# Optimization experiments

Measured on AMD Instinct MI355X. Metric: run time of the kernel, lower is better.

The kernel has to match this reference:

```python
import jax, jax.numpy as jnp
import numpy as np

B, K, D, S, E = 256, 512, 64, 100000, 20000  # batch, knowledge_n, low_dim, student_n, exer_n


def setup_inputs() -> dict:
    key = jax.random.key(0)
    ks = jax.random.split(key, 10)
    stu_id = jax.random.randint(ks[0], (B,), 0, S)
    exer_id = jax.random.randint(ks[1], (B,), 0, E)
    kn_emb = jax.random.uniform(ks[2], (B, K), dtype=jnp.float32)
    # learned parameters (xavier-ish scale)
    stu_table = jax.random.normal(ks[3], (S, D), dtype=jnp.float32) * 0.05
    exer_table = jax.random.normal(ks[4], (E, D), dtype=jnp.float32) * 0.05
    kn_table = jax.random.normal(ks[5], (K, D), dtype=jnp.float32) * 0.05
    W1 = jax.random.normal(ks[6], (K, K + D), dtype=jnp.float32) * (2.0 / (2 * K + D)) ** 0.5
    W2 = jax.random.normal(ks[7], (K, K + D), dtype=jnp.float32) * (2.0 / (2 * K + D)) ** 0.5
    W3 = jax.random.normal(ks[8], (1, K), dtype=jnp.float32) * (2.0 / (K + 1)) ** 0.5
    b3 = jnp.zeros((1,), dtype=jnp.float32)
    return {"stu_id": stu_id, "exer_id": exer_id, "kn_emb": kn_emb,
            "stu_table": stu_table, "exer_table": exer_table, "kn_table": kn_table,
            "W1": W1, "W2": W2, "W3": W3, "b3": b3}


def reference(stu_id, exer_id, kn_emb, stu_table, exer_table, kn_table, W1, W2, W3, b3):
    k = kn_table.shape[0]  # knowledge_n
    # sigmoid(stu_emb @ kn_table.T): (B, K) per-concept proficiency / difficulty
    stu = jax.nn.sigmoid(stu_table[stu_id] @ kn_table.T)
    exer = jax.nn.sigmoid(exer_table[exer_id] @ kn_table.T)
    # Linear on cat([repeated stu/exer vec, kn_vector]) decomposes: split W into
    # the first K columns (acting on the batch vector, constant over the K axis)
    # and the last D columns (acting on kn_table, constant over batch).
    pref = jax.nn.sigmoid((stu @ W1[:, :k].T)[:, None, :] + (kn_table @ W1[:, k:].T)[None, :, :])  # (B,K,K)
    diff = jax.nn.sigmoid((exer @ W2[:, :k].T)[:, None, :] + (kn_table @ W2[:, k:].T)[None, :, :])  # (B,K,K)
    o = jax.nn.sigmoid(jnp.einsum('bkn,n->bk', pref - diff, W3[0]) + b3)  # (B,K)
    sum_out = jnp.sum(o * kn_emb, axis=1, keepdims=True)  # (B,1)
    count = jnp.sum(kn_emb, axis=1, keepdims=True)
    return sum_out / count
```

## Files before the change

kernel.cpp:

```cpp
#include <hip/hip_runtime.h>

#define B_ 256
#define K_ 512
#define D_ 64
#define KD_ 576
#define LOG2E 1.44269504088896340736f

typedef float v2f __attribute__((ext_vector_type(2)));
typedef float v4f __attribute__((ext_vector_type(4)));
typedef short bf16x8 __attribute__((ext_vector_type(8)));
typedef float f32x16 __attribute__((ext_vector_type(16)));

#define ZERO16 {0.f,0.f,0.f,0.f,0.f,0.f,0.f,0.f,0.f,0.f,0.f,0.f,0.f,0.f,0.f,0.f}

__device__ __forceinline__ float fexp2(float x) {
#if __has_builtin(__builtin_amdgcn_exp2f)
    return __builtin_amdgcn_exp2f(x);
#else
    float r; asm("v_exp_f32 %0, %1" : "=v"(r) : "v"(x)); return r;
#endif
}
__device__ __forceinline__ float frcp(float x) {
#if __has_builtin(__builtin_amdgcn_rcpf)
    return __builtin_amdgcn_rcpf(x);
#else
    float r; asm("v_rcp_f32 %0, %1" : "=v"(r) : "v"(x)); return r;
#endif
}
__device__ __forceinline__ float fsig(float x) {
    return frcp(1.0f + fexp2(-LOG2E * x));
}
__device__ __forceinline__ ushort f2bf(float f) {
    union { float f; unsigned u; } v; v.f = f;
    return (ushort)((v.u + 0x7FFFu + ((v.u >> 16) & 1u)) >> 16);
}
__device__ __forceinline__ bf16x8 ldcvt8(const float* p) {
    float4 a = *(const float4*)p;
    float4 b = *(const float4*)(p + 4);
    bf16x8 r;
    r[0] = (short)f2bf(a.x); r[1] = (short)f2bf(a.y);
    r[2] = (short)f2bf(a.z); r[3] = (short)f2bf(a.w);
    r[4] = (short)f2bf(b.x); r[5] = (short)f2bf(b.y);
    r[6] = (short)f2bf(b.z); r[7] = (short)f2bf(b.w);
    return r;
}

__global__ void __launch_bounds__(256) kSF(const int* __restrict__ sid,
                                           const int* __restrict__ eid,
                                           const float* __restrict__ stu_t,
                                           const float* __restrict__ exer_t,
                                           const float* __restrict__ kn_t,
                                           const float* __restrict__ W1,
                                           const float* __restrict__ W2,
                                           ushort* __restrict__ Sbu,
                                           float* __restrict__ FT1,
                                           float* __restrict__ FT2) {
    __shared__ float shm[64 * 65];
    const int bid = blockIdx.x, t = threadIdx.x;
    const int l = t & 63, w = t >> 6;
    const int dk = (l >> 5) * 8;
    if (bid < 64) {
        const int tab = bid >> 5, bt = (bid >> 3) & 3, nt = bid & 7;
        const int b0 = bt * 64, n0 = nt * 64;
        const int brow = b0 + (w & 1) * 32 + (l & 31);
        const int ncol = n0 + (w >> 1) * 32 + (l & 31);
        const int id = (tab ? eid : sid)[brow];
        const float* ar = (tab ? exer_t : stu_t) + (size_t)id * D_;
        const float* br = kn_t + (size_t)ncol * D_;
        f32x16 acc = ZERO16;
#pragma unroll
        for (int kk = 0; kk < 4; kk++) {
            bf16x8 a = ldcvt8(ar + kk * 16 + dk);
            bf16x8 b = ldcvt8(br + kk * 16 + dk);
            acc = __builtin_amdgcn_mfma_f32_32x32x16_bf16(a, b, acc, 0, 0, 0);
        }
        ushort* So = Sbu + (size_t)tab * B_ * K_;
#pragma unroll
        for (int r = 0; r < 16; r++) {
            const int row = (r & 3) + 8 * (r >> 2) + 4 * (l >> 5);
            So[(size_t)(b0 + (w & 1) * 32 + row) * K_ + ncol] = f2bf(fsig(acc[r]));
        }
    } else {
        const int fid = bid - 64;
        const int mat = fid >> 6, kt = (fid >> 3) & 7, nt = fid & 7;
        const int k0 = kt * 64, n0 = nt * 64;
        const int krow = k0 + (w & 1) * 32 + (l & 31);
        const int ncol = n0 + (w >> 1) * 32 + (l & 31);
        const float* Wm = mat ? W2 : W1;
        const float* ar = kn_t + (size_t)krow * D_;
        const float* br = Wm + (size_t)ncol * KD_ + K_;
        f32x16 acc = ZERO16;
#pragma unroll
        for (int kk = 0; kk < 4; kk++) {
            bf16x8 a = ldcvt8(ar + kk * 16 + dk);
            bf16x8 b = ldcvt8(br + kk * 16 + dk);
            acc = __builtin_amdgcn_mfma_f32_32x32x16_bf16(a, b, acc, 0, 0, 0);
        }
        const int nl_ = (w >> 1) * 32 + (l & 31);
#pragma unroll
        for (int r = 0; r < 16; r++) {
            const int row = (r & 3) + 8 * (r >> 2) + 4 * (l >> 5);
            shm[nl_ * 65 + (w & 1) * 32 + row] = fexp2(-LOG2E * acc[r]);
        }
        __syncthreads();
        float* Fo = mat ? FT2 : FT1;
#pragma unroll
        for (int i = 0; i < 16; i++) {
            const int q = i * 256 + t;
            const int r_ = q >> 6, c_ = q & 63;
            Fo[(size_t)(n0 + r_) * K_ + k0 + c_] = shm[r_ * 65 + c_];
        }
    }
}

__global__ void __launch_bounds__(256) kE(const ushort* __restrict__ Sbu,
                                          const float* __restrict__ W1,
                                          const float* __restrict__ W2,
                                          float* __restrict__ E) {
    __shared__ float shm[4224];
    const int bid = blockIdx.x, t = threadIdx.x;
    const int l = t & 63, w = t >> 6;
    const int mat = bid >> 7, bt = (bid >> 4) & 7, nt = bid & 15;
    const int b0 = bt * 32, n0 = nt * 32;
    const int arow = b0 + (l & 31);
    const int nrow = n0 + (l & 31);
    const int koff = w * 128 + (l >> 5) * 8;
    const short* Sp = (const short*)Sbu + (size_t)(mat * B_ + arow) * K_ + koff;
    const float* Wp = (mat ? W2 : W1) + (size_t)nrow * KD_ + koff;
    f32x16 acc = ZERO16;
#pragma unroll
    for (int kk = 0; kk < 8; kk++) {
        bf16x8 a = *(const bf16x8*)(Sp + kk * 16);
        bf16x8 b = ldcvt8(Wp + kk * 16);
        acc = __builtin_amdgcn_mfma_f32_32x32x16_bf16(a, b, acc, 0, 0, 0);
    }
#pragma unroll
    for (int r = 0; r < 16; r++) {
        const int row = (r & 3) + 8 * (r >> 2) + 4 * (l >> 5);
        shm[w * 1056 + row * 33 + (l & 31)] = acc[r];
    }
    __syncthreads();
#pragma unroll
    for (int i = 0; i < 4; i++) {
        const int o = i * 256 + t;
        const int row = (o >> 5) & 31, col = o & 31;
        const float v = shm[row * 33 + col] + shm[1056 + row * 33 + col]
                      + shm[2112 + row * 33 + col] + shm[3168 + row * 33 + col];
        E[(size_t)mat * B_ * K_ + (size_t)(b0 + row) * K_ + n0 + col]
            = fexp2(-LOG2E * v);
    }
}

__global__ void __launch_bounds__(512) kMain(const float* __restrict__ FT1,
                                             const float* __restrict__ FT2,
                                             const float* __restrict__ Ebase,
                                             const float* __restrict__ W3,
                                             float* __restrict__ pPart) {
    __shared__ float es[2][32][20];
    __shared__ float w3s[32];
    __shared__ float sacc[4][64][20];
    const int t = threadIdx.x, l = t & 63, w = t >> 6;
    const int kg = blockIdx.x, bG = blockIdx.y, ns = blockIdx.z;
    const int b0 = bG * 16, n0 = ns * 32;
    const int k = kg * 256 + l * 4;

#pragma unroll
    for (int it = 0; it < 2; it++) {
        const int idx = it * 512 + t;
        const int mat = idx >> 9, r = idx & 511, bl = r >> 5, nl = r & 31;
        es[mat][nl][bl] = Ebase[(size_t)mat * B_ * K_ + (size_t)(b0 + bl) * K_ + n0 + nl];
    }
    if (t < 32) w3s[t] = W3[n0 + t];
    __syncthreads();

    const int bg = w & 3, nh = w >> 2;
    const int wb0 = bg * 4;
    const float* f1p = FT1 + (size_t)(n0 + nh * 16) * K_ + k;
    const float* f2p = FT2 + (size_t)(n0 + nh * 16) * K_ + k;

    v4f acc0 = {0.f,0.f,0.f,0.f}, acc1 = {0.f,0.f,0.f,0.f};
    v4f acc2 = {0.f,0.f,0.f,0.f}, acc3 = {0.f,0.f,0.f,0.f};

#pragma unroll 4
    for (int nl = 0; nl < 16; nl++) {
        const int n = nh * 16 + nl;
        const v4f f1 = *(const v4f*)(f1p + (size_t)nl * K_);
        const v4f f2 = *(const v4f*)(f2p + (size_t)nl * K_);
        const float w3n = w3s[n];
        const v4f e1 = *(const v4f*)&es[0][n][wb0];
        const v4f e2 = *(const v4f*)&es[1][n][wb0];
        {
            const v4f pd = e1.x * f1 + 1.0f, qd = e2.x * f2 + 1.0f;
            const v4f den = pd * qd;
            v4f rc; rc.x = frcp(den.x); rc.y = frcp(den.y);
            rc.z = frcp(den.z); rc.w = frcp(den.w);
            acc0 += ((qd - pd) * w3n) * rc;
        }
        {
            const v4f pd = e1.y * f1 + 1.0f, qd = e2.y * f2 + 1.0f;
            const v4f den = pd * qd;
            v4f rc; rc.x = frcp(den.x); rc.y = frcp(den.y);
            rc.z = frcp(den.z); rc.w = frcp(den.w);
            acc1 += ((qd - pd) * w3n) * rc;
        }
        {
            const v4f pd = e1.z * f1 + 1.0f, qd = e2.z * f2 + 1.0f;
            const v4f den = pd * qd;
            v4f rc; rc.x = frcp(den.x); rc.y = frcp(den.y);
            rc.z = frcp(den.z); rc.w = frcp(den.w);
            acc2 += ((qd - pd) * w3n) * rc;
        }
        {
            const v4f pd = e1.w * f1 + 1.0f, qd = e2.w * f2 + 1.0f;
            const v4f den = pd * qd;
            v4f rc; rc.x = frcp(den.x); rc.y = frcp(den.y);
            rc.z = frcp(den.z); rc.w = frcp(den.w);
            acc3 += ((qd - pd) * w3n) * rc;
        }
    }

    if (nh == 0) {
        *(v4f*)&sacc[bg][l][0]  = acc0;
        *(v4f*)&sacc[bg][l][4]  = acc1;
        *(v4f*)&sacc[bg][l][8]  = acc2;
        *(v4f*)&sacc[bg][l][12] = acc3;
    }
    __syncthreads();
    if (nh == 1) {
        const v4f o0 = acc0 + *(const v4f*)&sacc[bg][l][0];
        const v4f o1 = acc1 + *(const v4f*)&sacc[bg][l][4];
        const v4f o2 = acc2 + *(const v4f*)&sacc[bg][l][8];
        const v4f o3 = acc3 + *(const v4f*)&sacc[bg][l][12];
        float* po = pPart + ((size_t)ns * B_ + b0 + wb0) * K_ + k;
        *(v4f*)(po)          = o0;
        *(v4f*)(po + K_)     = o1;
        *(v4f*)(po + 2 * K_) = o2;
        *(v4f*)(po + 3 * K_) = o3;
    }
}

__global__ void __launch_bounds__(256) kFin(const float* __restrict__ pPart,
                                            const float* __restrict__ kn_emb,
                                            const float* __restrict__ b3,
                                            float* __restrict__ out) {
    const int t = threadIdx.x, l = t & 63, w = t >> 6;
    const int b = blockIdx.x * 4 + w;
    const float b3v = b3[0];
    const float* ke = kn_emb + (size_t)b * K_;
    float num = 0.f, den = 0.f;
#pragma unroll
    for (int c = 0; c < 8; c++) {
        const int kk = c * 64 + l;
        float sv = 0.f;
#pragma unroll
        for (int s = 0; s < 16; s++)
            sv += pPart[((size_t)s * B_ + b) * K_ + kk];
        const float kv = ke[kk];
        num = fmaf(fsig(sv + b3v), kv, num);
        den += kv;
    }
#pragma unroll
    for (int off = 32; off; off >>= 1) {
        num += __shfl_xor(num, off, 64);
        den += __shfl_xor(den, off, 64);
    }
    if (l == 0) out[b] = num / den;
}

extern "C" void kernel_launch(void* const* d_in, const int* in_sizes, int n_in,
                              void* d_out, int out_size, void* d_ws, size_t ws_size,
                              hipStream_t stream) {
    const int*   stu_id     = (const int*)d_in[0];
    const int*   exer_id    = (const int*)d_in[1];
    const float* kn_emb     = (const float*)d_in[2];
    const float* stu_table  = (const float*)d_in[3];
    const float* exer_table = (const float*)d_in[4];
    const float* kn_table   = (const float*)d_in[5];
    const float* W1         = (const float*)d_in[6];
    const float* W2         = (const float*)d_in[7];
    const float* W3         = (const float*)d_in[8];
    const float* b3         = (const float*)d_in[9];
    float* out = (float*)d_out;

    float* ws = (float*)d_ws;
    float* FT1   = ws;
    float* FT2   = FT1 + (size_t)K_ * K_;
    float* E     = FT2 + (size_t)K_ * K_;
    ushort* Sbu  = (ushort*)(E + 2 * (size_t)B_ * K_);
    float* pPart = (float*)(Sbu + 2 * (size_t)B_ * K_);

    kSF<<<192, 256, 0, stream>>>(stu_id, exer_id, stu_table, exer_table,
                                 kn_table, W1, W2, Sbu, FT1, FT2);
    kE<<<256, 256, 0, stream>>>(Sbu, W1, W2, E);
    kMain<<<dim3(2, 16, 16), 512, 0, stream>>>(FT1, FT2, E, W3, pPart);
    kFin<<<64, 256, 0, stream>>>(pPart, kn_emb, b3, out);
}
```

Before: 38.16 us.

## Rebalance kernels, retile main kernel over n, and share reciprocals

The FT-computation blocks move from the first kernel into the E kernel, so the tiny S kernel runs alone and the E kernel gets extra independent work. The main kernel is retiled to 8 batch rows by 64 n per block, with four wave groups splitting n and a three-way LDS reduction. This halves the number of partial sums that the final kernel has to read. Reciprocals are now computed in pairs, one rcp on a product followed by multiplies, which trades rcp throughput for a small risk to precision and overflow.

```diff
diff --git a/kernel.cpp b/kernel.cpp
--- a/kernel.cpp
+++ b/kernel.cpp
@@ -6,7 +6,6 @@
 #define KD_ 576
 #define LOG2E 1.44269504088896340736f
 
-typedef float v2f __attribute__((ext_vector_type(2)));
 typedef float v4f __attribute__((ext_vector_type(4)));
 typedef short bf16x8 __attribute__((ext_vector_type(8)));
 typedef float f32x16 __attribute__((ext_vector_type(16)));
@@ -45,28 +44,87 @@
     return r;
 }
 
-__global__ void __launch_bounds__(256) kSF(const int* __restrict__ sid,
-                                           const int* __restrict__ eid,
-                                           const float* __restrict__ stu_t,
-                                           const float* __restrict__ exer_t,
-                                           const float* __restrict__ kn_t,
-                                           const float* __restrict__ W1,
-                                           const float* __restrict__ W2,
-                                           ushort* __restrict__ Sbu,
-                                           float* __restrict__ FT1,
-                                           float* __restrict__ FT2) {
-    __shared__ float shm[64 * 65];
+__global__ void __launch_bounds__(256) kS(const int* __restrict__ sid,
+                                          const int* __restrict__ eid,
+                                          const float* __restrict__ stu_t,
+                                          const float* __restrict__ exer_t,
+                                          const float* __restrict__ kn_t,
+                                          ushort* __restrict__ Sbu) {
     const int bid = blockIdx.x, t = threadIdx.x;
     const int l = t & 63, w = t >> 6;
     const int dk = (l >> 5) * 8;
-    if (bid < 64) {
-        const int tab = bid >> 5, bt = (bid >> 3) & 3, nt = bid & 7;
-        const int b0 = bt * 64, n0 = nt * 64;
-        const int brow = b0 + (w & 1) * 32 + (l & 31);
+    const int tab = bid >> 5, bt = (bid >> 3) & 3, nt = bid & 7;
+    const int b0 = bt * 64, n0 = nt * 64;
+    const int brow = b0 + (w & 1) * 32 + (l & 31);
+    const int ncol = n0 + (w >> 1) * 32 + (l & 31);
+    const int id = (tab ? eid : sid)[brow];
+    const float* ar = (tab ? exer_t : stu_t) + (size_t)id * D_;
+    const float* br = kn_t + (size_t)ncol * D_;
+    f32x16 acc = ZERO16;
+#pragma unroll
+    for (int kk = 0; kk < 4; kk++) {
+        bf16x8 a = ldcvt8(ar + kk * 16 + dk);
+        bf16x8 b = ldcvt8(br + kk * 16 + dk);
+        acc = __builtin_amdgcn_mfma_f32_32x32x16_bf16(a, b, acc, 0, 0, 0);
+    }
+    ushort* So = Sbu + (size_t)tab * B_ * K_;
+#pragma unroll
+    for (int r = 0; r < 16; r++) {
+        const int row = (r & 3) + 8 * (r >> 2) + 4 * (l >> 5);
+        So[(size_t)(b0 + (w & 1) * 32 + row) * K_ + ncol] = f2bf(fsig(acc[r]));
+    }
+}
+
+__global__ void __launch_bounds__(256) kEF(const ushort* __restrict__ Sbu,
+                                           const float* __restrict__ W1,
+                                           const float* __restrict__ W2,
+                                           const float* __restrict__ kn_t,
+                                           float* __restrict__ E,
+                                           float* __restrict__ FT1,
+                                           float* __restrict__ FT2) {
+    __shared__ float shm[4224];
+    const int bid = blockIdx.x, t = threadIdx.x;
+    const int l = t & 63, w = t >> 6;
+    if (bid < 256) {
+        const int mat = bid >> 7, bt = (bid >> 4) & 7, nt = bid & 15;
+        const int b0 = bt * 32, n0 = nt * 32;
+        const int arow = b0 + (l & 31);
+        const int nrow = n0 + (l & 31);
+        const int koff = w * 128 + (l >> 5) * 8;
+        const short* Sp = (const short*)Sbu + (size_t)(mat * B_ + arow) * K_ + koff;
+        const float* Wp = (mat ? W2 : W1) + (size_t)nrow * KD_ + koff;
+        f32x16 acc = ZERO16;
+#pragma unroll
+        for (int kk = 0; kk < 8; kk++) {
+            bf16x8 a = *(const bf16x8*)(Sp + kk * 16);
+            bf16x8 b = ldcvt8(Wp + kk * 16);
+            acc = __builtin_amdgcn_mfma_f32_32x32x16_bf16(a, b, acc, 0, 0, 0);
+        }
+#pragma unroll
+        for (int r = 0; r < 16; r++) {
+            const int row = (r & 3) + 8 * (r >> 2) + 4 * (l >> 5);
+            shm[w * 1056 + row * 33 + (l & 31)] = acc[r];
+        }
+        __syncthreads();
+#pragma unroll
+        for (int i = 0; i < 4; i++) {
+            const int o = i * 256 + t;
+            const int row = (o >> 5) & 31, col = o & 31;
+            const float v = shm[row * 33 + col] + shm[1056 + row * 33 + col]
+                          + shm[2112 + row * 33 + col] + shm[3168 + row * 33 + col];
+            E[(size_t)mat * B_ * K_ + (size_t)(b0 + row) * K_ + n0 + col]
+                = fexp2(-LOG2E * v);
+        }
+    } else {
+        const int fid = bid - 256;
+        const int mat = fid >> 6, kt = (fid >> 3) & 7, nt = fid & 7;
+        const int k0 = kt * 64, n0 = nt * 64;
+        const int krow = k0 + (w & 1) * 32 + (l & 31);
         const int ncol = n0 + (w >> 1) * 32 + (l & 31);
-        const int id = (tab ? eid : sid)[brow];
-        const float* ar = (tab ? exer_t : stu_t) + (size_t)id * D_;
-        const float* br = kn_t + (size_t)ncol * D_;
+        const int dk = (l >> 5) * 8;
+        const float* Wm = mat ? W2 : W1;
+        const float* ar = kn_t + (size_t)krow * D_;
+        const float* br = Wm + (size_t)ncol * KD_ + K_;
         f32x16 acc = ZERO16;
 #pragma unroll
         for (int kk = 0; kk < 4; kk++) {
@@ -74,28 +132,6 @@
             bf16x8 b = ldcvt8(br + kk * 16 + dk);
             acc = __builtin_amdgcn_mfma_f32_32x32x16_bf16(a, b, acc, 0, 0, 0);
         }
-        ushort* So = Sbu + (size_t)tab * B_ * K_;
-#pragma unroll
-        for (int r = 0; r < 16; r++) {
-            const int row = (r & 3) + 8 * (r >> 2) + 4 * (l >> 5);
-            So[(size_t)(b0 + (w & 1) * 32 + row) * K_ + ncol] = f2bf(fsig(acc[r]));
-        }
-    } else {
-        const int fid = bid - 64;
-        const int mat = fid >> 6, kt = (fid >> 3) & 7, nt = fid & 7;
-        const int k0 = kt * 64, n0 = nt * 64;
-        const int krow = k0 + (w & 1) * 32 + (l & 31);
-        const int ncol = n0 + (w >> 1) * 32 + (l & 31);
-        const float* Wm = mat ? W2 : W1;
-        const float* ar = kn_t + (size_t)krow * D_;
-        const float* br = Wm + (size_t)ncol * KD_ + K_;
-        f32x16 acc = ZERO16;
-#pragma unroll
-        for (int kk = 0; kk < 4; kk++) {
-            bf16x8 a = ldcvt8(ar + kk * 16 + dk);
-            bf16x8 b = ldcvt8(br + kk * 16 + dk);
-            acc = __builtin_amdgcn_mfma_f32_32x32x16_bf16(a, b, acc, 0, 0, 0);
-        }
         const int nl_ = (w >> 1) * 32 + (l & 31);
 #pragma unroll
         for (int r = 0; r < 16; r++) {
@@ -110,44 +146,6 @@
             const int r_ = q >> 6, c_ = q & 63;
             Fo[(size_t)(n0 + r_) * K_ + k0 + c_] = shm[r_ * 65 + c_];
         }
-    }
-}
-
-__global__ void __launch_bounds__(256) kE(const ushort* __restrict__ Sbu,
-                                          const float* __restrict__ W1,
-                                          const float* __restrict__ W2,
-                                          float* __restrict__ E) {
-    __shared__ float shm[4224];
-    const int bid = blockIdx.x, t = threadIdx.x;
-    const int l = t & 63, w = t >> 6;
-    const int mat = bid >> 7, bt = (bid >> 4) & 7, nt = bid & 15;
-    const int b0 = bt * 32, n0 = nt * 32;
-    const int arow = b0 + (l & 31);
-    const int nrow = n0 + (l & 31);
-    const int koff = w * 128 + (l >> 5) * 8;
-    const short* Sp = (const short*)Sbu + (size_t)(mat * B_ + arow) * K_ + koff;
-    const float* Wp = (mat ? W2 : W1) + (size_t)nrow * KD_ + koff;
-    f32x16 acc = ZERO16;
-#pragma unroll
-    for (int kk = 0; kk < 8; kk++) {
-        bf16x8 a = *(const bf16x8*)(Sp + kk * 16);
-        bf16x8 b = ldcvt8(Wp + kk * 16);
-        acc = __builtin_amdgcn_mfma_f32_32x32x16_bf16(a, b, acc, 0, 0, 0);
-    }
-#pragma unroll
-    for (int r = 0; r < 16; r++) {
-        const int row = (r & 3) + 8 * (r >> 2) + 4 * (l >> 5);
-        shm[w * 1056 + row * 33 + (l & 31)] = acc[r];
-    }
-    __syncthreads();
-#pragma unroll
-    for (int i = 0; i < 4; i++) {
-        const int o = i * 256 + t;
-        const int row = (o >> 5) & 31, col = o & 31;
-        const float v = shm[row * 33 + col] + shm[1056 + row * 33 + col]
-                      + shm[2112 + row * 33 + col] + shm[3168 + row * 33 + col];
-        E[(size_t)mat * B_ * K_ + (size_t)(b0 + row) * K_ + n0 + col]
-            = fexp2(-LOG2E * v);
     }
 }
 
@@ -156,86 +154,73 @@
                                              const float* __restrict__ Ebase,
                                              const float* __restrict__ W3,
                                              float* __restrict__ pPart) {
-    __shared__ float es[2][32][20];
-    __shared__ float w3s[32];
-    __shared__ float sacc[4][64][20];
+    __shared__ float es[2][64][8];
+    __shared__ float sacc[3][2][16][64];
     const int t = threadIdx.x, l = t & 63, w = t >> 6;
     const int kg = blockIdx.x, bG = blockIdx.y, ns = blockIdx.z;
-    const int b0 = bG * 16, n0 = ns * 32;
+    const int b0 = bG * 8, n0 = ns * 64;
     const int k = kg * 256 + l * 4;
+    const int bh = w & 1, nq = w >> 1;
 
 #pragma unroll
     for (int it = 0; it < 2; it++) {
-        const int idx = it * 512 + t;
-        const int mat = idx >> 9, r = idx & 511, bl = r >> 5, nl = r & 31;
-        es[mat][nl][bl] = Ebase[(size_t)mat * B_ * K_ + (size_t)(b0 + bl) * K_ + n0 + nl];
-    }
-    if (t < 32) w3s[t] = W3[n0 + t];
+        const int i = it * 512 + t;
+        const int n = i & 63, b = (i >> 6) & 7, mat = i >> 9;
+        es[mat][n][b] = Ebase[(size_t)mat * B_ * K_ + (size_t)(b0 + b) * K_ + n0 + n];
+    }
     __syncthreads();
 
-    const int bg = w & 3, nh = w >> 2;
-    const int wb0 = bg * 4;
-    const float* f1p = FT1 + (size_t)(n0 + nh * 16) * K_ + k;
-    const float* f2p = FT2 + (size_t)(n0 + nh * 16) * K_ + k;
-
-    v4f acc0 = {0.f,0.f,0.f,0.f}, acc1 = {0.f,0.f,0.f,0.f};
-    v4f acc2 = {0.f,0.f,0.f,0.f}, acc3 = {0.f,0.f,0.f,0.f};
+    const float* f1p = FT1 + (size_t)(n0 + nq * 16) * K_ + k;
+    const float* f2p = FT2 + (size_t)(n0 + nq * 16) * K_ + k;
+    const float* w3p = W3 + n0 + nq * 16;
+
+    v4f acc[4];
+#pragma unroll
+    for (int b = 0; b < 4; b++) acc[b] = (v4f){0.f, 0.f, 0.f, 0.f};
 
 #pragma unroll 4
     for (int nl = 0; nl < 16; nl++) {
-        const int n = nh * 16 + nl;
         const v4f f1 = *(const v4f*)(f1p + (size_t)nl * K_);
         const v4f f2 = *(const v4f*)(f2p + (size_t)nl * K_);
-        const float w3n = w3s[n];
-        const v4f e1 = *(const v4f*)&es[0][n][wb0];
-        const v4f e2 = *(const v4f*)&es[1][n][wb0];
-        {
-            const v4f pd = e1.x * f1 + 1.0f, qd = e2.x * f2 + 1.0f;
+        const float w3n = w3p[nl];
+        const v4f e1 = *(const v4f*)&es[0][nq * 16 + nl][bh * 4];
+        const v4f e2 = *(const v4f*)&es[1][nq * 16 + nl][bh * 4];
+#pragma unroll
+        for (int b = 0; b < 4; b++) {
+            const v4f pd = e1[b] * f1 + 1.0f;
+            const v4f qd = e2[b] * f2 + 1.0f;
             const v4f den = pd * qd;
-            v4f rc; rc.x = frcp(den.x); rc.y = frcp(den.y);
-            rc.z = frcp(den.z); rc.w = frcp(den.w);
-            acc0 += ((qd - pd) * w3n) * rc;
-        }
-        {
-            const v4f pd = e1.y * f1 + 1.0f, qd = e2.y * f2 + 1.0f;
-            const v4f den = pd * qd;
-            v4f rc; rc.x = frcp(den.x); rc.y = frcp(den.y);
-            rc.z = frcp(den.z); rc.w = frcp(den.w);
-            acc1 += ((qd - pd) * w3n) * rc;
-        }
-        {
-            const v4f pd = e1.z * f1 + 1.0f, qd = e2.z * f2 + 1.0f;
-            const v4f den = pd * qd;
-            v4f rc; rc.x = frcp(den.x); rc.y = frcp(den.y);
-            rc.z = frcp(den.z); rc.w = frcp(den.w);
-            acc2 += ((qd - pd) * w3n) * rc;
-        }
-        {
-            const v4f pd = e1.w * f1 + 1.0f, qd = e2.w * f2 + 1.0f;
-            const v4f den = pd * qd;
-            v4f rc; rc.x = frcp(den.x); rc.y = frcp(den.y);
-            rc.z = frcp(den.z); rc.w = frcp(den.w);
-            acc3 += ((qd - pd) * w3n) * rc;
-        }
-    }
-
-    if (nh == 0) {
-        *(v4f*)&sacc[bg][l][0]  = acc0;
-        *(v4f*)&sacc[bg][l][4]  = acc1;
-        *(v4f*)&sacc[bg][l][8]  = acc2;
-        *(v4f*)&sacc[bg][l][12] = acc3;
+            const v4f num = (qd - pd) * w3n;
+            const float dxy = den.x * den.y, dzw = den.z * den.w;
+            const float rxy = frcp(dxy), rzw = frcp(dzw);
+            v4f rc;
+            rc.x = rxy * den.y; rc.y = rxy * den.x;
+            rc.z = rzw * den.w; rc.w = rzw * den.z;
+            acc[b] += num * rc;
+        }
+    }
+
+    if (nq != 0) {
+#pragma unroll
+        for (int b = 0; b < 4; b++)
+#pragma unroll
+            for (int c = 0; c < 4; c++)
+                sacc[nq - 1][bh][b * 4 + c][l] = acc[b][c];
     }
     __syncthreads();
-    if (nh == 1) {
-        const v4f o0 = acc0 + *(const v4f*)&sacc[bg][l][0];
-        const v4f o1 = acc1 + *(const v4f*)&sacc[bg][l][4];
-        const v4f o2 = acc2 + *(const v4f*)&sacc[bg][l][8];
-        const v4f o3 = acc3 + *(const v4f*)&sacc[bg][l][12];
-        float* po = pPart + ((size_t)ns * B_ + b0 + wb0) * K_ + k;
-        *(v4f*)(po)          = o0;
-        *(v4f*)(po + K_)     = o1;
-        *(v4f*)(po + 2 * K_) = o2;
-        *(v4f*)(po + 3 * K_) = o3;
+    if (nq == 0) {
+#pragma unroll
+        for (int b = 0; b < 4; b++) {
+            v4f s = acc[b];
+#pragma unroll
+            for (int q = 0; q < 3; q++) {
+                s.x += sacc[q][bh][b * 4 + 0][l];
+                s.y += sacc[q][bh][b * 4 + 1][l];
+                s.z += sacc[q][bh][b * 4 + 2][l];
+                s.w += sacc[q][bh][b * 4 + 3][l];
+            }
+            *(v4f*)(pPart + ((size_t)ns * B_ + b0 + bh * 4 + b) * K_ + k) = s;
+        }
     }
 }
 
@@ -253,7 +238,7 @@
         const int kk = c * 64 + l;
         float sv = 0.f;
 #pragma unroll
-        for (int s = 0; s < 16; s++)
+        for (int s = 0; s < 8; s++)
             sv += pPart[((size_t)s * B_ + b) * K_ + kk];
         const float kv = ke[kk];
         num = fmaf(fsig(sv + b3v), kv, num);
@@ -289,9 +274,9 @@
     ushort* Sbu  = (ushort*)(E + 2 * (size_t)B_ * K_);
     float* pPart = (float*)(Sbu + 2 * (size_t)B_ * K_);
 
-    kSF<<<192, 256, 0, stream>>>(stu_id, exer_id, stu_table, exer_table,
-                                 kn_table, W1, W2, Sbu, FT1, FT2);
-    kE<<<256, 256, 0, stream>>>(Sbu, W1, W2, E);
-    kMain<<<dim3(2, 16, 16), 512, 0, stream>>>(FT1, FT2, E, W3, pPart);
+    kS<<<64, 256, 0, stream>>>(stu_id, exer_id, stu_table, exer_table,
+                               kn_table, Sbu);
+    kEF<<<384, 256, 0, stream>>>(Sbu, W1, W2, kn_table, E, FT1, FT2);
+    kMain<<<dim3(2, 32, 8), 512, 0, stream>>>(FT1, FT2, E, W3, pPart);
     kFin<<<64, 256, 0, stream>>>(pPart, kn_emb, b3, out);
 }
```

Result: faster. 37.19 us (-2.5%).
